# Optimization experiments

Hardware: AMD Instinct MI355X
Metric: run time of the kernel (lower is better)

Reference implementation:

```python
import jax, jax.numpy as jnp
import numpy as np

B, S_SRC, S_TRG = 128, 512, 128
VIN, VOUT = 128, 128
E, H = 128, 256          # embed, encoder hidden
HD = 2 * H               # decoder hidden = 512 (concat of bi-dir encoder states)
DENC = 2 * H             # encoder output feature dim = 512


def setup_inputs() -> dict:
    key = jax.random.key(0)
    ks = jax.random.split(key, 20)
    g = lambda k, shape: (jax.random.normal(k, shape, jnp.float32) * 0.05)
    inp = {
        "src": jax.random.randint(ks[0], (B, S_SRC), 0, VIN, jnp.int32),
        "trg": jax.random.randint(ks[1], (B, S_TRG), 0, VOUT, jnp.int32),
        # encoder
        "enc_emb": g(ks[2], (VIN, E)),
        "enc_Wih_f": g(ks[3], (4 * H, E)),
        "enc_Whh_f": g(ks[4], (4 * H, H)),
        "enc_b_f": g(ks[5], (4 * H,)),
        "enc_Wih_b": g(ks[6], (4 * H, E)),
        "enc_Whh_b": g(ks[7], (4 * H, H)),
        "enc_b_b": g(ks[8], (4 * H,)),
        # decoder
        "dec_emb": g(ks[9], (VOUT, E)),
        "dec_Wih": g(ks[10], (4 * HD, E + DENC)),
        "dec_Whh": g(ks[11], (4 * HD, HD)),
        "dec_b": g(ks[12], (4 * HD,)),
        # attention: Linear(dec_hid + enc_dim -> HD), v: Linear(HD -> 1)
        "attn_W": g(ks[13], (HD + DENC, HD)),
        "attn_b": g(ks[14], (HD,)),
        "attn_v": g(ks[15], (HD,)),
        # output projection
        "out_W": g(ks[16], (HD, VOUT)),
        "out_b": g(ks[17], (VOUT,)),
    }
    return inp


def _lstm_cell(h, c, x, Wih, Whh, b):
    gates = x @ Wih.T + h @ Whh.T + b               # [B, 4H]
    i, f, gg, o = jnp.split(gates, 4, axis=-1)       # PyTorch gate order i,f,g,o
    i, f, o = jax.nn.sigmoid(i), jax.nn.sigmoid(f), jax.nn.sigmoid(o)
    c = f * c + i * jnp.tanh(gg)
    h = o * jnp.tanh(c)
    return h, c


def _lstm_scan(xs, Wih, Whh, b, reverse=False):
    # xs: [S, B, E] -> hs: [S, B, H] (time-aligned), plus final (h, c)
    Bn, Hn = xs.shape[1], Whh.shape[1]
    init = (jnp.zeros((Bn, Hn), xs.dtype), jnp.zeros((Bn, Hn), xs.dtype))
    def step(carry, x):
        h, c = _lstm_cell(carry[0], carry[1], x, Wih, Whh, b)
        return (h, c), h
    (h, c), hs = jax.lax.scan(step, init, xs, reverse=reverse)
    return hs, h, c


def reference(src, trg, enc_emb, enc_Wih_f, enc_Whh_f, enc_b_f,
              enc_Wih_b, enc_Whh_b, enc_b_b, dec_emb, dec_Wih, dec_Whh,
              dec_b, attn_W, attn_b, attn_v, out_W, out_b):
    # ----- encoder (bidirectional LSTM) -----
    emb = enc_emb[src]                                # [B, S, E]
    xs = jnp.swapaxes(emb, 0, 1)                      # [S, B, E]
    hs_f, hf, cf = _lstm_scan(xs, enc_Wih_f, enc_Whh_f, enc_b_f, reverse=False)
    hs_b, hb, cb = _lstm_scan(xs, enc_Wih_b, enc_Whh_b, enc_b_b, reverse=True)
    enc_out = jnp.swapaxes(jnp.concatenate([hs_f, hs_b], -1), 0, 1)  # [B, S, 2H]
    hidden = jnp.concatenate([hf, hb], -1)            # [B, HD]  (hidden.view(1,B,-1))
    cell = jnp.concatenate([cf, cb], -1)              # [B, HD]

    # attention linear split: energy = tanh([h, enc] @ W + b)
    Wh, We = attn_W[:HD], attn_W[HD:]
    enc_proj = jnp.einsum("bsd,de->bse", enc_out, We)  # [B, S, HD] precomputed

    def dec_step(carry, tok):
        h, c = carry
        e = jnp.tanh(h[:, None, :] @ Wh + enc_proj + attn_b)     # [B, S, HD]
        scores = jnp.einsum("bse,e->bs", e, attn_v)              # [B, S]
        aw = jax.nn.softmax(scores, axis=1)
        ctx = jnp.einsum("bs,bsd->bd", aw, enc_out)              # [B, DENC]
        x = jnp.concatenate([dec_emb[tok], ctx], -1)             # [B, E+DENC]
        h, c = _lstm_cell(h, c, x, dec_Wih, dec_Whh, dec_b)
        logits = h @ out_W + out_b                               # [B, VOUT]
        return (h, c), logits

    # teacher forcing (ratio=1.0): input at step t is trg[:, t-1], t = 1..T-1
    toks = jnp.swapaxes(trg[:, :-1], 0, 1)            # [T-1, B]
    _, logits = jax.lax.scan(dec_step, (hidden, cell), toks)
    logits = jnp.swapaxes(logits, 0, 1)               # [B, T-1, VOUT]
    outputs = jnp.concatenate(
        [jnp.zeros((src.shape[0], 1, VOUT), logits.dtype), logits], axis=1)
    return outputs
```

## Files before the change

### kernel.cpp

```cpp
#include <hip/hip_runtime.h>


typedef _Float16 f16;
typedef _Float16 half8 __attribute__((ext_vector_type(8)));
typedef float f32x4 __attribute__((ext_vector_type(4)));
typedef char char8v __attribute__((ext_vector_type(8)));

#define MFMA16(a, b, c) __builtin_amdgcn_mfma_f32_16x16x32_f16((a), (b), (c), 0, 0, 0)

#define PSCALE (2.5f / 127.f)
#define PINV   (127.f / 2.5f)

__device__ __forceinline__ float fsig(float x) {
    return __builtin_amdgcn_rcpf(1.f + __expf(-x));
}
__device__ __forceinline__ float ftanh(float x) {
    return 1.f - 2.f * __builtin_amdgcn_rcpf(1.f + __expf(2.f * x));
}
__device__ __forceinline__ int frag_idx(int m, int k, int KS) {
    return (((m >> 4) * KS + (k >> 5)) * 64 + (((k >> 3) & 3) * 16 + (m & 15))) * 8 + (k & 7);
}

__global__ __launch_bounds__(256) void k_prep(
    const float* __restrict__ attn_W, const float* __restrict__ out_W,
    const float* __restrict__ enc_emb,
    const float* __restrict__ wihf, const float* __restrict__ wihb,
    const float* __restrict__ whhf, const float* __restrict__ whhb,
    const float* __restrict__ dec_emb, const float* __restrict__ dec_wih,
    const float* __restrict__ dec_whh,
    f16* __restrict__ WhT_sw, f16* __restrict__ outWT_sw,
    f16* __restrict__ whhf_sw, f16* __restrict__ whhb_sw,
    f16* __restrict__ decwih_sw, f16* __restrict__ decwhh_sw,
    f16* __restrict__ WeT, f16* __restrict__ emb16,
    f16* __restrict__ wihf16, f16* __restrict__ wihb16,
    f16* __restrict__ decemb16, float* __restrict__ out)
{
    long i = (long)blockIdx.x * 256 + threadIdx.x;
    if (i >= 3784704L) return;
    long idx = i;
    if (idx < 262144) {
        int j = idx & 7, lane = (idx >> 3) & 63, c = lane & 15, q = lane >> 4;
        int ks = (idx >> 9) & 15, nt = idx >> 13;
        WhT_sw[idx] = (f16)attn_W[(ks * 32 + q * 8 + j) * 512 + nt * 16 + c];
        return;
    }
    idx -= 262144;
    if (idx < 65536) {
        int j = idx & 7, lane = (idx >> 3) & 63, c = lane & 15, q = lane >> 4;
        int ks = (idx >> 9) & 15, nt = idx >> 13;
        outWT_sw[idx] = (f16)out_W[(ks * 32 + q * 8 + j) * 128 + nt * 16 + c];
        return;
    }
    idx -= 65536;
    if (idx < 262144) {
        int j = idx & 7, lane = (idx >> 3) & 63, c = lane & 15, q = lane >> 4;
        int ks = (idx >> 9) & 7, nt = idx >> 12;
        whhf_sw[idx] = (f16)whhf[(nt * 16 + c) * 256 + ks * 32 + q * 8 + j];
        return;
    }
    idx -= 262144;
    if (idx < 262144) {
        int j = idx & 7, lane = (idx >> 3) & 63, c = lane & 15, q = lane >> 4;
        int ks = (idx >> 9) & 7, nt = idx >> 12;
        whhb_sw[idx] = (f16)whhb[(nt * 16 + c) * 256 + ks * 32 + q * 8 + j];
        return;
    }
    idx -= 262144;
    if (idx < 1310720) {
        int j = idx & 7, lane = (idx >> 3) & 63, c = lane & 15, q = lane >> 4;
        int r2 = idx >> 9; int ks = r2 % 20, nt = r2 / 20;
        decwih_sw[idx] = (f16)dec_wih[(nt * 16 + c) * 640 + ks * 32 + q * 8 + j];
        return;
    }
    idx -= 1310720;
    if (idx < 1048576) {
        int j = idx & 7, lane = (idx >> 3) & 63, c = lane & 15, q = lane >> 4;
        int ks = (idx >> 9) & 15, nt = idx >> 13;
        decwhh_sw[idx] = (f16)dec_whh[(nt * 16 + c) * 512 + ks * 32 + q * 8 + j];
        return;
    }
    idx -= 1048576;
    if (idx < 262144) { int e = idx >> 9, d = idx & 511; WeT[idx] = (f16)attn_W[(512 + d) * 512 + e]; return; }
    idx -= 262144;
    if (idx < 16384)  { emb16[idx] = (f16)enc_emb[idx]; return; }
    idx -= 16384;
    if (idx < 131072) { wihf16[idx] = (f16)wihf[idx]; return; }
    idx -= 131072;
    if (idx < 131072) { wihb16[idx] = (f16)wihb[idx]; return; }
    idx -= 131072;
    if (idx < 16384)  { decemb16[idx] = (f16)dec_emb[idx]; return; }
    idx -= 16384;
    if (idx < 16384)  { int b = idx >> 7, v = idx & 127; out[b * 16384 + v] = 0.f; return; }
}

__global__ __launch_bounds__(256) void k_vocab(
    const f16* __restrict__ emb, const f16* __restrict__ wihf,
    const f16* __restrict__ wihb, const float* __restrict__ bf_,
    const float* __restrict__ bb_, f16* __restrict__ xg_vocab)
{
    int bn = blockIdx.x;
    int tid = threadIdx.x, wave = tid >> 6, lane = tid & 63;
    int col = lane & 15, quad = lane >> 4;
    int wr = wave >> 1, wc = wave & 1;

    f32x4 acc[4][4] = {};
    for (int ks = 0; ks < 4; ++ks) {
        int k0 = ks * 32 + quad * 8;
        half8 a[4], bfr[4];
        for (int i = 0; i < 4; ++i)
            a[i] = *(const half8*)(emb + (wr * 64 + i * 16 + col) * 128 + k0);
        for (int j = 0; j < 4; ++j) {
            int n = bn * 128 + wc * 64 + j * 16 + col;
            const f16* wp = (n < 1024) ? (wihf + n * 128) : (wihb + (n - 1024) * 128);
            bfr[j] = *(const half8*)(wp + k0);
        }
        for (int i = 0; i < 4; ++i)
            for (int j = 0; j < 4; ++j)
                acc[i][j] = MFMA16(a[i], bfr[j], acc[i][j]);
    }
    for (int j = 0; j < 4; ++j) {
        int n = bn * 128 + wc * 64 + j * 16 + col;
        float bias = (n < 1024) ? bf_[n] : bb_[n - 1024];
        for (int i = 0; i < 4; ++i) {
            int vbase = wr * 64 + i * 16 + quad * 4;
            for (int r = 0; r < 4; ++r)
                xg_vocab[(vbase + r) * 2048 + n] = (f16)(acc[i][j][r] + bias);
        }
    }
}

__global__ __launch_bounds__(512, 2) void k_enc(
    const int* __restrict__ src, const f16* __restrict__ xg_vocab,
    const f16* __restrict__ whhf_sw, const f16* __restrict__ whhb_sw,
    f16* __restrict__ enc_out, f16* __restrict__ hdec0, float* __restrict__ c_ws)
{
    int blk = blockIdx.x;
    int dir = blk >> 3, bbase = (blk & 7) * 16;
    int tid = threadIdx.x, wave = tid >> 6, lane = tid & 63;
    int col = lane & 15, quad = lane >> 4;
    const f16* whh = dir ? whhb_sw : whhf_sw;

    __shared__ f16 hb[16][264];
    __shared__ f16 xvb[16][1032];
    __shared__ int stok[16];
    for (int z = tid; z < 16 * 264; z += 512) ((f16*)hb)[z] = (f16)0.f;
    float cc[2][4] = {};

    half8 bst[32];
    #pragma unroll
    for (int g = 0; g < 2; ++g)
        #pragma unroll
        for (int nt = 0; nt < 2; ++nt)
            #pragma unroll
            for (int kk = 0; kk < 8; ++kk) {
                int tile = g * 16 + wave * 2 + nt;
                bst[(g * 2 + nt) * 8 + kk] =
                    *(const half8*)(whh + ((tile * 8 + kk) * 64 + lane) * 8);
            }
    __syncthreads();

    for (int t = 0; t < 512; ++t) {
        int ts = dir ? (511 - t) : t;
        if (tid < 16) stok[tid] = src[(bbase + tid) * 512 + ts];
        half8 a[8];
        #pragma unroll
        for (int kk = 0; kk < 8; ++kk)
            a[kk] = *(const half8*)(&hb[col][kk * 32 + quad * 8]);
        __syncthreads();

        #pragma unroll
        for (int it = 0; it < 4; ++it) {
            int cnk = it * 512 + tid;
            int row = cnk >> 7, off = (cnk & 127) * 8;
            *(half8*)(&xvb[row][off]) =
                *(const half8*)(xg_vocab + stok[row] * 2048 + dir * 1024 + off);
        }

        f32x4 acc[4][2] = {};
        #pragma unroll
        for (int kk = 0; kk < 8; ++kk) {
            half8 bv[4];
            #pragma unroll
            for (int g = 2; g < 4; ++g)
                #pragma unroll
                for (int nt = 0; nt < 2; ++nt) {
                    int tile = g * 16 + wave * 2 + nt;
                    bv[(g - 2) * 2 + nt] =
                        *(const half8*)(whh + ((tile * 8 + kk) * 64 + lane) * 8);
                }
            #pragma unroll
            for (int g = 0; g < 2; ++g)
                #pragma unroll
                for (int nt = 0; nt < 2; ++nt)
                    acc[g][nt] = MFMA16(a[kk], bst[(g * 2 + nt) * 8 + kk], acc[g][nt]);
            #pragma unroll
            for (int g = 2; g < 4; ++g)
                #pragma unroll
                for (int nt = 0; nt < 2; ++nt)
                    acc[g][nt] = MFMA16(a[kk], bv[(g - 2) * 2 + nt], acc[g][nt]);
        }
        __syncthreads();

        #pragma unroll
        for (int nt = 0; nt < 2; ++nt) {
            int hcol = wave * 32 + nt * 16 + col;
            #pragma unroll
            for (int r = 0; r < 4; ++r) {
                int b = quad * 4 + r;
                float gi = (float)xvb[b][0 * 256 + hcol] + acc[0][nt][r];
                float gf = (float)xvb[b][1 * 256 + hcol] + acc[1][nt][r];
                float gg = (float)xvb[b][2 * 256 + hcol] + acc[2][nt][r];
                float go = (float)xvb[b][3 * 256 + hcol] + acc[3][nt][r];
                float ig = fsig(gi), fg = fsig(gf), g2 = ftanh(gg), og = fsig(go);
                float cv = fg * cc[nt][r] + ig * g2;
                cc[nt][r] = cv;
                float h = og * ftanh(cv);
                f16 h16 = (f16)h;
                hb[b][hcol] = h16;
                enc_out[((size_t)(bbase + b) * 512 + ts) * 512 + dir * 256 + hcol] = h16;
            }
        }
        __syncthreads();
    }
    #pragma unroll
    for (int nt = 0; nt < 2; ++nt) {
        int hcol = wave * 32 + nt * 16 + col;
        #pragma unroll
        for (int r = 0; r < 4; ++r) {
            int b = quad * 4 + r;
            int m = bbase + b, k = dir * 256 + hcol;
            hdec0[frag_idx(m, k, 16)] = hb[b][hcol];
            c_ws[m * 512 + k] = cc[nt][r];
        }
    }
}

__global__ __launch_bounds__(256) void k_proj(
    const f16* __restrict__ enc_out, const f16* __restrict__ WeT,
    char* __restrict__ proj8)
{
    int blk = blockIdx.x;
    int bm = blk & 511, bn = blk >> 9;
    int tid = threadIdx.x, wave = tid >> 6, lane = tid & 63;
    int col = lane & 15, quad = lane >> 4;
    int wr = wave >> 1, wc = wave & 1;

    f32x4 acc[4][4] = {};
    for (int ks = 0; ks < 16; ++ks) {
        int k0 = ks * 32 + quad * 8;
        half8 a[4], bfr[4];
        for (int i = 0; i < 4; ++i) {
            int m = bm * 128 + wr * 64 + i * 16 + col;
            a[i] = *(const half8*)(enc_out + (size_t)m * 512 + k0);
        }
        for (int j = 0; j < 4; ++j) {
            int n = bn * 128 + wc * 64 + j * 16 + col;
            bfr[j] = *(const half8*)(WeT + n * 512 + k0);
        }
        for (int i = 0; i < 4; ++i)
            for (int j = 0; j < 4; ++j)
                acc[i][j] = MFMA16(a[i], bfr[j], acc[i][j]);
    }
    for (int j = 0; j < 4; ++j) {
        int n = bn * 128 + wc * 64 + j * 16 + col;
        for (int i = 0; i < 4; ++i) {
            int mbase = bm * 128 + wr * 64 + i * 16 + quad * 4;
            for (int r = 0; r < 4; ++r) {
                float v = acc[i][j][r] * PINV;
                int q = (int)rintf(v);
                q = (q > 127) ? 127 : ((q < -127) ? -127 : q);
                proj8[(size_t)(mbase + r) * 512 + n] = (char)q;
            }
        }
    }
}

__global__ __launch_bounds__(256) void k_qinit(
    const f16* __restrict__ h0_sw, const f16* __restrict__ WhT_sw,
    float* __restrict__ qpart)
{
    int j = blockIdx.x;
    int tid = threadIdx.x, wave = tid >> 6, lane = tid & 63;
    int col = lane & 15, quad = lane >> 4;
    half8 a[2];
    #pragma unroll
    for (int i = 0; i < 2; ++i)
        a[i] = *(const half8*)(h0_sw + (((wave * 2 + i) * 16 + j) * 64 + lane) * 8);
    for (int nt = 0; nt < 32; ++nt) {
        half8 bfr = *(const half8*)(WhT_sw + ((nt * 16 + j) * 64 + lane) * 8);
        f32x4 q0 = {}, q1 = {};
        q0 = MFMA16(a[0], bfr, q0);
        q1 = MFMA16(a[1], bfr, q1);
        #pragma unroll
        for (int r = 0; r < 4; ++r) {
            qpart[(j * 128 + wave * 32 + quad * 4 + r) * 512 + nt * 16 + col] = q0[r];
            qpart[(j * 128 + wave * 32 + 16 + quad * 4 + r) * 512 + nt * 16 + col] = q1[r];
        }
    }
}

__global__ __launch_bounds__(512) void k_att(
    const char* __restrict__ proj8, const f16* __restrict__ enc_out,
    const float* __restrict__ qpart, const float* __restrict__ attn_b,
    const float* __restrict__ attn_v, const int* __restrict__ trg,
    const f16* __restrict__ dec_emb, f16* __restrict__ x_sw,
    float* __restrict__ part_m, float* __restrict__ part_l,
    float* __restrict__ part_ctx, int t)
{
    int blk = blockIdx.x;
    int b = blk >> 1, sh = blk & 1;
    int tid = threadIdx.x, wave = tid >> 6, lane = tid & 63;
    __shared__ float q[512];
    __shared__ float sc[256];
    __shared__ float ctxred[8][512];
    __shared__ float wred[8], wred2[8];

    {
        float s = attn_b[tid];
        #pragma unroll
        for (int jj = 0; jj < 16; ++jj) s += qpart[(jj * 128 + b) * 512 + tid];
        q[tid] = s;
    }
    __syncthreads();

    float qreg[8], vreg[8];
    #pragma unroll
    for (int u = 0; u < 8; ++u) {
        int e = lane * 8 + u;
        qreg[u] = q[e];
        vreg[u] = attn_v[e];
    }
    int sbase = sh * 256;
    for (int ib = 0; ib < 4; ++ib) {
        char8v p[8];
        #pragma unroll
        for (int z = 0; z < 8; ++z) {
            int sl = (ib * 8 + z) * 8 + wave;
            p[z] = *(const char8v*)(proj8 + ((size_t)b * 512 + sbase + sl) * 512 + lane * 8);
        }
        #pragma unroll
        for (int z = 0; z < 8; ++z) {
            int sl = (ib * 8 + z) * 8 + wave;
            float part = 0.f;
            #pragma unroll
            for (int u = 0; u < 8; ++u)
                part += vreg[u] * ftanh(fmaf((float)p[z][u], PSCALE, qreg[u]));
            #pragma unroll
            for (int o = 32; o; o >>= 1) part += __shfl_xor(part, o);
            if (lane == 0) sc[sl] = part;
        }
    }
    __syncthreads();

    float s0 = (tid < 256) ? sc[tid] : -__builtin_inff();
    float mv = s0;
    #pragma unroll
    for (int o = 32; o; o >>= 1) mv = fmaxf(mv, __shfl_xor(mv, o));
    if (lane == 0) wred[wave] = mv;
    __syncthreads();
    float M = wred[0];
    #pragma unroll
    for (int w = 1; w < 8; ++w) M = fmaxf(M, wred[w]);
    float e0 = (tid < 256) ? __expf(s0 - M) : 0.f;
    if (tid < 256) sc[tid] = e0;
    float sm = e0;
    #pragma unroll
    for (int o = 32; o; o >>= 1) sm += __shfl_xor(sm, o);
    if (lane == 0) wred2[wave] = sm;
    __syncthreads();
    float lb = wred2[0];
    #pragma unroll
    for (int w = 1; w < 8; ++w) lb += wred2[w];

    float a8[8] = {};
    for (int ib = 0; ib < 4; ++ib) {
        half8 ev[8];
        float wgt[8];
        #pragma unroll
        for (int z = 0; z < 8; ++z) {
            int sl = (ib * 8 + z) * 8 + wave;
            ev[z] = *(const half8*)(enc_out + ((size_t)b * 512 + sbase + sl) * 512 + lane * 8);
            wgt[z] = sc[sl];
        }
        #pragma unroll
        for (int z = 0; z < 8; ++z)
            #pragma unroll
            for (int u = 0; u < 8; ++u) a8[u] += wgt[z] * (float)ev[z][u];
    }
    #pragma unroll
    for (int u = 0; u < 8; ++u) ctxred[wave][lane * 8 + u] = a8[u];
    __syncthreads();
    float cp = 0.f;
    #pragma unroll
    for (int w = 0; w < 8; ++w) cp += ctxred[w][tid];
    part_ctx[(size_t)blk * 512 + tid] = cp;
    if (tid == 0) { part_m[blk] = M; part_l[blk] = lb; }

    if (sh == 0 && tid < 128) {
        int tok = trg[b * 128 + t];
        x_sw[frag_idx(b, tid, 20)] = dec_emb[tok * 128 + tid];
    }
}

__global__ __launch_bounds__(256) void k_gates(
    f16* __restrict__ x_sw, const f16* __restrict__ hprev_sw,
    const f16* __restrict__ wih_sw, const f16* __restrict__ whh_sw,
    const float* __restrict__ dec_b, float* __restrict__ c_ws,
    f16* __restrict__ hnext_sw, f16* __restrict__ hhist_sw,
    const f16* __restrict__ WhT_sw, float* __restrict__ qpart,
    const float* __restrict__ part_m, const float* __restrict__ part_l,
    const float* __restrict__ part_ctx, int t)
{
    int jb = blockIdx.x;
    int j = jb >> 1, mh = jb & 1;
    int tid = threadIdx.x, wave = tid >> 6, lane = tid & 63;
    int col = lane & 15, quad = lane >> 4;
    __shared__ f16 hsl[64][40];
    __shared__ float gm[64][2];

    if (tid < 64) {
        int bb = mh * 64 + tid;
        float m0 = part_m[bb * 2 + 0], m1 = part_m[bb * 2 + 1];
        float l0 = part_l[bb * 2 + 0], l1 = part_l[bb * 2 + 1];
        float M = fmaxf(m0, m1);
        float g0 = __expf(m0 - M), g1 = __expf(m1 - M);
        float inv = 1.f / (g0 * l0 + g1 * l1);
        gm[tid][0] = g0 * inv;
        gm[tid][1] = g1 * inv;
    }
    __syncthreads();
    for (int z = tid; z < 32768; z += 256) {
        int lr = z >> 9, d = z & 511;
        int bb = mh * 64 + lr;
        float c = gm[lr][0] * part_ctx[(size_t)(bb * 2 + 0) * 512 + d]
                + gm[lr][1] * part_ctx[(size_t)(bb * 2 + 1) * 512 + d];
        x_sw[frag_idx(bb, 128 + d, 20)] = (f16)c;
    }
    __syncthreads();

    f32x4 acc[8] = {};
    for (int ks = 0; ks < 36; ++ks) {
        int mtile = mh * 4 + wave;
        half8 a = (ks < 20)
            ? *(const half8*)(x_sw + ((mtile * 20 + ks) * 64 + lane) * 8)
            : *(const half8*)(hprev_sw + ((mtile * 16 + (ks - 20)) * 64 + lane) * 8);
        half8 bv[8];
        #pragma unroll
        for (int jt = 0; jt < 8; ++jt) {
            int g = jt >> 1, u2 = jt & 1;
            int ntile = g * 32 + j * 2 + u2;
            bv[jt] = (ks < 20)
                ? *(const half8*)(wih_sw + ((ntile * 20 + ks) * 64 + lane) * 8)
                : *(const half8*)(whh_sw + ((ntile * 16 + (ks - 20)) * 64 + lane) * 8);
        }
        #pragma unroll
        for (int jt = 0; jt < 8; ++jt)
            acc[jt] = MFMA16(a, bv[jt], acc[jt]);
    }
    float bias[8];
    #pragma unroll
    for (int jt = 0; jt < 8; ++jt) {
        int g = jt >> 1, u2 = jt & 1;
        bias[jt] = dec_b[g * 512 + j * 32 + u2 * 16 + col];
    }
    #pragma unroll
    for (int r = 0; r < 4; ++r) {
        int lb = wave * 16 + quad * 4 + r;
        int bb = mh * 64 + lb;
        #pragma unroll
        for (int u2 = 0; u2 < 2; ++u2) {
            int hl = u2 * 16 + col, hcol = j * 32 + hl;
            float gi = acc[0 + u2][r] + bias[0 + u2];
            float gf = acc[2 + u2][r] + bias[2 + u2];
            float gg = acc[4 + u2][r] + bias[4 + u2];
            float go = acc[6 + u2][r] + bias[6 + u2];
            float ig = fsig(gi), fg = fsig(gf), g2 = ftanh(gg), og = fsig(go);
            float cv = fg * c_ws[bb * 512 + hcol] + ig * g2;
            c_ws[bb * 512 + hcol] = cv;
            float h = og * ftanh(cv);
            f16 h16 = (f16)h;
            int fidx = frag_idx(bb, hcol, 16);
            hnext_sw[fidx] = h16;
            hhist_sw[t * 65536 + fidx] = h16;
            hsl[lb][hl] = h16;
        }
    }
    half8 aq = *(const half8*)(&hsl[wave * 16 + col][quad * 8]);
    for (int nt = 0; nt < 32; ++nt) {
        half8 bq = *(const half8*)(WhT_sw + ((nt * 16 + j) * 64 + lane) * 8);
        f32x4 q0 = {};
        q0 = MFMA16(aq, bq, q0);
        #pragma unroll
        for (int r = 0; r < 4; ++r)
            qpart[(j * 128 + mh * 64 + wave * 16 + quad * 4 + r) * 512 + nt * 16 + col] = q0[r];
    }
}

__global__ __launch_bounds__(256) void k_logits(
    const f16* __restrict__ hhist_sw, const f16* __restrict__ outWT_sw,
    const float* __restrict__ out_b, float* __restrict__ out)
{
    int bt = blockIdx.x;
    int tid = threadIdx.x, wave = tid >> 6, lane = tid & 63;
    int col = lane & 15, quad = lane >> 4;
    f32x4 acc[2][8] = {};
    for (int ks = 0; ks < 16; ++ks) {
        half8 a[2];
        #pragma unroll
        for (int i = 0; i < 2; ++i)
            a[i] = *(const half8*)(hhist_sw + bt * 65536 + (((wave * 2 + i) * 16 + ks) * 64 + lane) * 8);
        half8 bv[8];
        #pragma unroll
        for (int jt = 0; jt < 8; ++jt)
            bv[jt] = *(const half8*)(outWT_sw + ((jt * 16 + ks) * 64 + lane) * 8);
        #pragma unroll
        for (int jt = 0; jt < 8; ++jt) {
            acc[0][jt] = MFMA16(a[0], bv[jt], acc[0][jt]);
            acc[1][jt] = MFMA16(a[1], bv[jt], acc[1][jt]);
        }
    }
    #pragma unroll
    for (int jt = 0; jt < 8; ++jt) {
        float bias = out_b[jt * 16 + col];
        #pragma unroll
        for (int i = 0; i < 2; ++i)
            #pragma unroll
            for (int r = 0; r < 4; ++r) {
                int br = wave * 32 + i * 16 + quad * 4 + r;
                out[br * 16384 + (bt + 1) * 128 + jt * 16 + col] = acc[i][jt][r] + bias;
            }
    }
}

extern "C" void kernel_launch(void* const* d_in, const int* in_sizes, int n_in,
                              void* d_out, int out_size, void* d_ws, size_t ws_size,
                              hipStream_t stream)
{
    (void)in_sizes; (void)n_in; (void)out_size;
    if (ws_size < 130000000) return;

    const int*   src     = (const int*)d_in[0];
    const int*   trg     = (const int*)d_in[1];
    const float* enc_emb = (const float*)d_in[2];
    const float* wihf    = (const float*)d_in[3];
    const float* whhf    = (const float*)d_in[4];
    const float* bf_     = (const float*)d_in[5];
    const float* wihb    = (const float*)d_in[6];
    const float* whhb    = (const float*)d_in[7];
    const float* bb_     = (const float*)d_in[8];
    const float* dec_emb = (const float*)d_in[9];
    const float* dec_wih = (const float*)d_in[10];
    const float* dec_whh = (const float*)d_in[11];
    const float* dec_b   = (const float*)d_in[12];
    const float* attn_W  = (const float*)d_in[13];
    const float* attn_b  = (const float*)d_in[14];
    const float* attn_v  = (const float*)d_in[15];
    const float* out_W   = (const float*)d_in[16];
    const float* out_b   = (const float*)d_in[17];
    float* out = (float*)d_out;

    char* p = (char*)d_ws;
    auto carve = [&](size_t n) { char* r = p; p += ((n + 255) & ~(size_t)255); return r; };
    f16*   enc_out   = (f16*)  carve(67108864);
    char*  proj8     = (char*) carve(33554432);
    f16*   WhT_sw    = (f16*)  carve(524288);
    f16*   WeT       = (f16*)  carve(524288);
    f16*   outWT_sw  = (f16*)  carve(131072);
    f16*   emb16     = (f16*)  carve(32768);
    f16*   wihf16    = (f16*)  carve(262144);
    f16*   wihb16    = (f16*)  carve(262144);
    f16*   whhf_sw   = (f16*)  carve(524288);
    f16*   whhb_sw   = (f16*)  carve(524288);
    f16*   decemb16  = (f16*)  carve(32768);
    f16*   decwih_sw = (f16*)  carve(2621440);
    f16*   decwhh_sw = (f16*)  carve(2097152);
    float* qpart     = (float*)carve(4194304);
    f16*   hdec0     = (f16*)  carve(131072);
    f16*   hdec1     = (f16*)  carve(131072);
    float* c_ws      = (float*)carve(262144);
    f16*   x_sw      = (f16*)  carve(163840);
    f16*   hhist_sw  = (f16*)  carve(16646144);
    f16*   xg_vocab  = (f16*)  carve(524288);
    float* part_m    = (float*)carve(2048);
    float* part_l    = (float*)carve(2048);
    float* part_ctx  = (float*)carve(524288);

    k_prep<<<14784, 256, 0, stream>>>(attn_W, out_W, enc_emb, wihf, wihb, whhf, whhb,
                                      dec_emb, dec_wih, dec_whh,
                                      WhT_sw, outWT_sw, whhf_sw, whhb_sw,
                                      decwih_sw, decwhh_sw, WeT, emb16,
                                      wihf16, wihb16, decemb16, out);
    k_vocab<<<16, 256, 0, stream>>>(emb16, wihf16, wihb16, bf_, bb_, xg_vocab);
    k_enc<<<16, 512, 0, stream>>>(src, xg_vocab, whhf_sw, whhb_sw, enc_out, hdec0, c_ws);
    k_proj<<<2048, 256, 0, stream>>>(enc_out, WeT, proj8);
    k_qinit<<<16, 256, 0, stream>>>(hdec0, WhT_sw, qpart);
    for (int t = 0; t < 127; ++t) {
        k_att<<<256, 512, 0, stream>>>(proj8, enc_out, qpart, attn_b, attn_v,
                                       trg, decemb16, x_sw, part_m, part_l,
                                       part_ctx, t);
        f16* hin  = (t & 1) ? hdec1 : hdec0;
        f16* hout = (t & 1) ? hdec0 : hdec1;
        k_gates<<<32, 256, 0, stream>>>(x_sw, hin, decwih_sw, decwhh_sw, dec_b,
                                        c_ws, hout, hhist_sw, WhT_sw, qpart,
                                        part_m, part_l, part_ctx, t);
    }
    k_logits<<<127, 256, 0, stream>>>(hhist_sw, outWT_sw, out_b, out);
}
```

Baseline: 13.06 ms.

## Fuse decoder attention and gate kernels into one persistent kernel with grid barriers

```diff
diff --git a/kernel.cpp b/kernel.cpp
--- a/kernel.cpp
+++ b/kernel.cpp
@@ -19,6 +19,23 @@
 }
 __device__ __forceinline__ int frag_idx(int m, int k, int KS) {
     return (((m >> 4) * KS + (k >> 5)) * 64 + (((k >> 3) & 3) * 16 + (m & 15))) * 8 + (k & 7);
+}
+
+__device__ __forceinline__ void gridbar(int* cnt, int* gen, int nblk) {
+    __syncthreads();
+    if (threadIdx.x == 0) {
+        int g = __hip_atomic_load(gen, __ATOMIC_RELAXED, __HIP_MEMORY_SCOPE_AGENT);
+        int v = __hip_atomic_fetch_add(cnt, 1, __ATOMIC_RELEASE, __HIP_MEMORY_SCOPE_AGENT);
+        if (v == nblk - 1) {
+            __hip_atomic_store(cnt, 0, __ATOMIC_RELAXED, __HIP_MEMORY_SCOPE_AGENT);
+            __hip_atomic_fetch_add(gen, 1, __ATOMIC_RELEASE, __HIP_MEMORY_SCOPE_AGENT);
+        } else {
+            while (__hip_atomic_load(gen, __ATOMIC_RELAXED, __HIP_MEMORY_SCOPE_AGENT) == g)
+                __builtin_amdgcn_s_sleep(2);
+        }
+        __builtin_amdgcn_fence(__ATOMIC_ACQUIRE, "agent");
+    }
+    __syncthreads();
 }
 
 __global__ __launch_bounds__(256) void k_prep(
@@ -33,10 +50,11 @@
     f16* __restrict__ decwih_sw, f16* __restrict__ decwhh_sw,
     f16* __restrict__ WeT, f16* __restrict__ emb16,
     f16* __restrict__ wihf16, f16* __restrict__ wihb16,
-    f16* __restrict__ decemb16, float* __restrict__ out)
+    f16* __restrict__ decemb16, float* __restrict__ out,
+    int* __restrict__ syncb)
 {
     long i = (long)blockIdx.x * 256 + threadIdx.x;
-    if (i >= 3784704L) return;
+    if (i >= 3784768L) return;
     long idx = i;
     if (idx < 262144) {
         int j = idx & 7, lane = (idx >> 3) & 63, c = lane & 15, q = lane >> 4;
@@ -91,6 +109,8 @@
     if (idx < 16384)  { decemb16[idx] = (f16)dec_emb[idx]; return; }
     idx -= 16384;
     if (idx < 16384)  { int b = idx >> 7, v = idx & 127; out[b * 16384 + v] = 0.f; return; }
+    idx -= 16384;
+    if (idx < 64)     { syncb[idx] = 0; return; }
 }
 
 __global__ __launch_bounds__(256) void k_vocab(
@@ -299,200 +319,211 @@
     }
 }
 
-__global__ __launch_bounds__(512) void k_att(
+__global__ __launch_bounds__(512, 2) void k_dec(
     const char* __restrict__ proj8, const f16* __restrict__ enc_out,
-    const float* __restrict__ qpart, const float* __restrict__ attn_b,
+    float* __restrict__ qpart, const float* __restrict__ attn_b,
     const float* __restrict__ attn_v, const int* __restrict__ trg,
-    const f16* __restrict__ dec_emb, f16* __restrict__ x_sw,
+    const f16* __restrict__ decemb, f16* __restrict__ x_sw,
+    const f16* __restrict__ wih_sw, const f16* __restrict__ whh_sw,
+    const float* __restrict__ dec_b, float* __restrict__ c_ws,
+    f16* __restrict__ hd0, f16* __restrict__ hd1, f16* __restrict__ hhist_sw,
+    const f16* __restrict__ WhT_sw,
     float* __restrict__ part_m, float* __restrict__ part_l,
-    float* __restrict__ part_ctx, int t)
+    float* __restrict__ part_ctx, int* __restrict__ syncb)
 {
     int blk = blockIdx.x;
     int b = blk >> 1, sh = blk & 1;
     int tid = threadIdx.x, wave = tid >> 6, lane = tid & 63;
+    int col = lane & 15, quad = lane >> 4;
+    int nblk = gridDim.x;
+    int* cnt = syncb;
+    int* gen = syncb + 16;
+
     __shared__ float q[512];
     __shared__ float sc[256];
     __shared__ float ctxred[8][512];
     __shared__ float wred[8], wred2[8];
-
-    {
-        float s = attn_b[tid];
-        #pragma unroll
-        for (int jj = 0; jj < 16; ++jj) s += qpart[(jj * 128 + b) * 512 + tid];
-        q[tid] = s;
-    }
-    __syncthreads();
-
-    float qreg[8], vreg[8];
-    #pragma unroll
-    for (int u = 0; u < 8; ++u) {
-        int e = lane * 8 + u;
-        qreg[u] = q[e];
-        vreg[u] = attn_v[e];
-    }
-    int sbase = sh * 256;
-    for (int ib = 0; ib < 4; ++ib) {
-        char8v p[8];
-        #pragma unroll
-        for (int z = 0; z < 8; ++z) {
-            int sl = (ib * 8 + z) * 8 + wave;
-            p[z] = *(const char8v*)(proj8 + ((size_t)b * 512 + sbase + sl) * 512 + lane * 8);
-        }
-        #pragma unroll
-        for (int z = 0; z < 8; ++z) {
-            int sl = (ib * 8 + z) * 8 + wave;
-            float part = 0.f;
-            #pragma unroll
-            for (int u = 0; u < 8; ++u)
-                part += vreg[u] * ftanh(fmaf((float)p[z][u], PSCALE, qreg[u]));
-            #pragma unroll
-            for (int o = 32; o; o >>= 1) part += __shfl_xor(part, o);
-            if (lane == 0) sc[sl] = part;
-        }
-    }
-    __syncthreads();
-
-    float s0 = (tid < 256) ? sc[tid] : -__builtin_inff();
-    float mv = s0;
-    #pragma unroll
-    for (int o = 32; o; o >>= 1) mv = fmaxf(mv, __shfl_xor(mv, o));
-    if (lane == 0) wred[wave] = mv;
-    __syncthreads();
-    float M = wred[0];
-    #pragma unroll
-    for (int w = 1; w < 8; ++w) M = fmaxf(M, wred[w]);
-    float e0 = (tid < 256) ? __expf(s0 - M) : 0.f;
-    if (tid < 256) sc[tid] = e0;
-    float sm = e0;
-    #pragma unroll
-    for (int o = 32; o; o >>= 1) sm += __shfl_xor(sm, o);
-    if (lane == 0) wred2[wave] = sm;
-    __syncthreads();
-    float lb = wred2[0];
-    #pragma unroll
-    for (int w = 1; w < 8; ++w) lb += wred2[w];
-
-    float a8[8] = {};
-    for (int ib = 0; ib < 4; ++ib) {
-        half8 ev[8];
-        float wgt[8];
-        #pragma unroll
-        for (int z = 0; z < 8; ++z) {
-            int sl = (ib * 8 + z) * 8 + wave;
-            ev[z] = *(const half8*)(enc_out + ((size_t)b * 512 + sbase + sl) * 512 + lane * 8);
-            wgt[z] = sc[sl];
-        }
-        #pragma unroll
-        for (int z = 0; z < 8; ++z)
-            #pragma unroll
-            for (int u = 0; u < 8; ++u) a8[u] += wgt[z] * (float)ev[z][u];
-    }
-    #pragma unroll
-    for (int u = 0; u < 8; ++u) ctxred[wave][lane * 8 + u] = a8[u];
-    __syncthreads();
-    float cp = 0.f;
-    #pragma unroll
-    for (int w = 0; w < 8; ++w) cp += ctxred[w][tid];
-    part_ctx[(size_t)blk * 512 + tid] = cp;
-    if (tid == 0) { part_m[blk] = M; part_l[blk] = lb; }
-
-    if (sh == 0 && tid < 128) {
-        int tok = trg[b * 128 + t];
-        x_sw[frag_idx(b, tid, 20)] = dec_emb[tok * 128 + tid];
-    }
-}
-
-__global__ __launch_bounds__(256) void k_gates(
-    f16* __restrict__ x_sw, const f16* __restrict__ hprev_sw,
-    const f16* __restrict__ wih_sw, const f16* __restrict__ whh_sw,
-    const float* __restrict__ dec_b, float* __restrict__ c_ws,
-    f16* __restrict__ hnext_sw, f16* __restrict__ hhist_sw,
-    const f16* __restrict__ WhT_sw, float* __restrict__ qpart,
-    const float* __restrict__ part_m, const float* __restrict__ part_l,
-    const float* __restrict__ part_ctx, int t)
-{
-    int jb = blockIdx.x;
-    int j = jb >> 1, mh = jb & 1;
-    int tid = threadIdx.x, wave = tid >> 6, lane = tid & 63;
-    int col = lane & 15, quad = lane >> 4;
     __shared__ f16 hsl[64][40];
     __shared__ float gm[64][2];
 
-    if (tid < 64) {
-        int bb = mh * 64 + tid;
-        float m0 = part_m[bb * 2 + 0], m1 = part_m[bb * 2 + 1];
-        float l0 = part_l[bb * 2 + 0], l1 = part_l[bb * 2 + 1];
-        float M = fmaxf(m0, m1);
-        float g0 = __expf(m0 - M), g1 = __expf(m1 - M);
-        float inv = 1.f / (g0 * l0 + g1 * l1);
-        gm[tid][0] = g0 * inv;
-        gm[tid][1] = g1 * inv;
-    }
-    __syncthreads();
-    for (int z = tid; z < 32768; z += 256) {
-        int lr = z >> 9, d = z & 511;
-        int bb = mh * 64 + lr;
-        float c = gm[lr][0] * part_ctx[(size_t)(bb * 2 + 0) * 512 + d]
-                + gm[lr][1] * part_ctx[(size_t)(bb * 2 + 1) * 512 + d];
-        x_sw[frag_idx(bb, 128 + d, 20)] = (f16)c;
-    }
-    __syncthreads();
-
-    f32x4 acc[8] = {};
-    for (int ks = 0; ks < 36; ++ks) {
-        int mtile = mh * 4 + wave;
-        half8 a = (ks < 20)
-            ? *(const half8*)(x_sw + ((mtile * 20 + ks) * 64 + lane) * 8)
-            : *(const half8*)(hprev_sw + ((mtile * 16 + (ks - 20)) * 64 + lane) * 8);
-        half8 bv[8];
+    int gj = blk >> 1, gmh = blk & 1;
+    float bias[8];
+    if (blk < 32) {
         #pragma unroll
         for (int jt = 0; jt < 8; ++jt) {
             int g = jt >> 1, u2 = jt & 1;
-            int ntile = g * 32 + j * 2 + u2;
-            bv[jt] = (ks < 20)
-                ? *(const half8*)(wih_sw + ((ntile * 20 + ks) * 64 + lane) * 8)
-                : *(const half8*)(whh_sw + ((ntile * 16 + (ks - 20)) * 64 + lane) * 8);
-        }
-        #pragma unroll
-        for (int jt = 0; jt < 8; ++jt)
-            acc[jt] = MFMA16(a, bv[jt], acc[jt]);
-    }
-    float bias[8];
+            bias[jt] = dec_b[g * 512 + gj * 32 + u2 * 16 + col];
+        }
+    }
+    float vreg[8];
     #pragma unroll
-    for (int jt = 0; jt < 8; ++jt) {
-        int g = jt >> 1, u2 = jt & 1;
-        bias[jt] = dec_b[g * 512 + j * 32 + u2 * 16 + col];
-    }
-    #pragma unroll
-    for (int r = 0; r < 4; ++r) {
-        int lb = wave * 16 + quad * 4 + r;
-        int bb = mh * 64 + lb;
-        #pragma unroll
-        for (int u2 = 0; u2 < 2; ++u2) {
-            int hl = u2 * 16 + col, hcol = j * 32 + hl;
-            float gi = acc[0 + u2][r] + bias[0 + u2];
-            float gf = acc[2 + u2][r] + bias[2 + u2];
-            float gg = acc[4 + u2][r] + bias[4 + u2];
-            float go = acc[6 + u2][r] + bias[6 + u2];
-            float ig = fsig(gi), fg = fsig(gf), g2 = ftanh(gg), og = fsig(go);
-            float cv = fg * c_ws[bb * 512 + hcol] + ig * g2;
-            c_ws[bb * 512 + hcol] = cv;
-            float h = og * ftanh(cv);
-            f16 h16 = (f16)h;
-            int fidx = frag_idx(bb, hcol, 16);
-            hnext_sw[fidx] = h16;
-            hhist_sw[t * 65536 + fidx] = h16;
-            hsl[lb][hl] = h16;
-        }
-    }
-    half8 aq = *(const half8*)(&hsl[wave * 16 + col][quad * 8]);
-    for (int nt = 0; nt < 32; ++nt) {
-        half8 bq = *(const half8*)(WhT_sw + ((nt * 16 + j) * 64 + lane) * 8);
-        f32x4 q0 = {};
-        q0 = MFMA16(aq, bq, q0);
-        #pragma unroll
-        for (int r = 0; r < 4; ++r)
-            qpart[(j * 128 + mh * 64 + wave * 16 + quad * 4 + r) * 512 + nt * 16 + col] = q0[r];
+    for (int u = 0; u < 8; ++u) vreg[u] = attn_v[lane * 8 + u];
+    int sbase = sh * 256;
+
+    for (int t = 0; t < 127; ++t) {
+        {
+            float s = attn_b[tid];
+            #pragma unroll
+            for (int jj = 0; jj < 16; ++jj) s += qpart[(jj * 128 + b) * 512 + tid];
+            q[tid] = s;
+        }
+        __syncthreads();
+
+        float qreg[8];
+        #pragma unroll
+        for (int u = 0; u < 8; ++u) qreg[u] = q[lane * 8 + u];
+
+        for (int ib = 0; ib < 4; ++ib) {
+            char8v p[8];
+            #pragma unroll
+            for (int z = 0; z < 8; ++z) {
+                int sl = (ib * 8 + z) * 8 + wave;
+                p[z] = *(const char8v*)(proj8 + ((size_t)b * 512 + sbase + sl) * 512 + lane * 8);
+            }
+            #pragma unroll
+            for (int z = 0; z < 8; ++z) {
+                int sl = (ib * 8 + z) * 8 + wave;
+                float part = 0.f;
+                #pragma unroll
+                for (int u = 0; u < 8; ++u)
+                    part += vreg[u] * ftanh(fmaf((float)p[z][u], PSCALE, qreg[u]));
+                #pragma unroll
+                for (int o = 32; o; o >>= 1) part += __shfl_xor(part, o);
+                if (lane == 0) sc[sl] = part;
+            }
+        }
+        __syncthreads();
+
+        float s0 = (tid < 256) ? sc[tid] : -__builtin_inff();
+        float mv = s0;
+        #pragma unroll
+        for (int o = 32; o; o >>= 1) mv = fmaxf(mv, __shfl_xor(mv, o));
+        if (lane == 0) wred[wave] = mv;
+        __syncthreads();
+        float M = wred[0];
+        #pragma unroll
+        for (int w = 1; w < 8; ++w) M = fmaxf(M, wred[w]);
+        float e0 = (tid < 256) ? __expf(s0 - M) : 0.f;
+        if (tid < 256) sc[tid] = e0;
+        float sm = e0;
+        #pragma unroll
+        for (int o = 32; o; o >>= 1) sm += __shfl_xor(sm, o);
+        if (lane == 0) wred2[wave] = sm;
+        __syncthreads();
+        float lb2 = wred2[0];
+        #pragma unroll
+        for (int w = 1; w < 8; ++w) lb2 += wred2[w];
+
+        float a8[8] = {};
+        for (int ib = 0; ib < 4; ++ib) {
+            half8 ev[8];
+            float wgt[8];
+            #pragma unroll
+            for (int z = 0; z < 8; ++z) {
+                int sl = (ib * 8 + z) * 8 + wave;
+                ev[z] = *(const half8*)(enc_out + ((size_t)b * 512 + sbase + sl) * 512 + lane * 8);
+                wgt[z] = sc[sl];
+            }
+            #pragma unroll
+            for (int z = 0; z < 8; ++z)
+                #pragma unroll
+                for (int u = 0; u < 8; ++u) a8[u] += wgt[z] * (float)ev[z][u];
+        }
+        #pragma unroll
+        for (int u = 0; u < 8; ++u) ctxred[wave][lane * 8 + u] = a8[u];
+        __syncthreads();
+        float cp = 0.f;
+        #pragma unroll
+        for (int w = 0; w < 8; ++w) cp += ctxred[w][tid];
+        part_ctx[(size_t)blk * 512 + tid] = cp;
+        if (tid == 0) { part_m[blk] = M; part_l[blk] = lb2; }
+
+        if (sh == 0 && tid < 128) {
+            int tok = trg[b * 128 + t];
+            x_sw[frag_idx(b, tid, 20)] = decemb[tok * 128 + tid];
+        }
+
+        gridbar(cnt, gen, nblk);
+
+        if (blk < 32 && tid < 64) {
+            int bb = gmh * 64 + tid;
+            float m0 = part_m[bb * 2 + 0], m1 = part_m[bb * 2 + 1];
+            float l0 = part_l[bb * 2 + 0], l1 = part_l[bb * 2 + 1];
+            float Mx = fmaxf(m0, m1);
+            float g0 = __expf(m0 - Mx), g1 = __expf(m1 - Mx);
+            float inv = 1.f / (g0 * l0 + g1 * l1);
+            gm[tid][0] = g0 * inv;
+            gm[tid][1] = g1 * inv;
+        }
+        __syncthreads();
+        if (blk < 32) {
+            for (int z = tid; z < 32768; z += 512) {
+                int lr = z >> 9, d = z & 511;
+                int bb = gmh * 64 + lr;
+                float c = gm[lr][0] * part_ctx[(size_t)(bb * 2 + 0) * 512 + d]
+                        + gm[lr][1] * part_ctx[(size_t)(bb * 2 + 1) * 512 + d];
+                x_sw[frag_idx(bb, 128 + d, 20)] = (f16)c;
+            }
+        }
+        __syncthreads();
+
+        if (blk < 32 && wave < 4) {
+            const f16* hprev = (t & 1) ? hd1 : hd0;
+            f16* hnext = (t & 1) ? hd0 : hd1;
+
+            f32x4 acc[8] = {};
+            for (int ks = 0; ks < 36; ++ks) {
+                int mtile = gmh * 4 + wave;
+                half8 a = (ks < 20)
+                    ? *(const half8*)(x_sw + ((mtile * 20 + ks) * 64 + lane) * 8)
+                    : *(const half8*)(hprev + ((mtile * 16 + (ks - 20)) * 64 + lane) * 8);
+                half8 bv[8];
+                #pragma unroll
+                for (int jt = 0; jt < 8; ++jt) {
+                    int g = jt >> 1, u2 = jt & 1;
+                    int ntile = g * 32 + gj * 2 + u2;
+                    bv[jt] = (ks < 20)
+                        ? *(const half8*)(wih_sw + ((ntile * 20 + ks) * 64 + lane) * 8)
+                        : *(const half8*)(whh_sw + ((ntile * 16 + (ks - 20)) * 64 + lane) * 8);
+                }
+                #pragma unroll
+                for (int jt = 0; jt < 8; ++jt)
+                    acc[jt] = MFMA16(a, bv[jt], acc[jt]);
+            }
+            #pragma unroll
+            for (int r = 0; r < 4; ++r) {
+                int lr = wave * 16 + quad * 4 + r;
+                int bb = gmh * 64 + lr;
+                #pragma unroll
+                for (int u2 = 0; u2 < 2; ++u2) {
+                    int hl = u2 * 16 + col, hcol = gj * 32 + hl;
+                    float gi = acc[0 + u2][r] + bias[0 + u2];
+                    float gf = acc[2 + u2][r] + bias[2 + u2];
+                    float gg = acc[4 + u2][r] + bias[4 + u2];
+                    float go = acc[6 + u2][r] + bias[6 + u2];
+                    float ig = fsig(gi), fg = fsig(gf), g2 = ftanh(gg), og = fsig(go);
+                    float cv = fg * c_ws[bb * 512 + hcol] + ig * g2;
+                    c_ws[bb * 512 + hcol] = cv;
+                    float h = og * ftanh(cv);
+                    f16 h16 = (f16)h;
+                    int fidx = frag_idx(bb, hcol, 16);
+                    hnext[fidx] = h16;
+                    hhist_sw[t * 65536 + fidx] = h16;
+                    hsl[lr][hl] = h16;
+                }
+            }
+            half8 aq = *(const half8*)(&hsl[wave * 16 + col][quad * 8]);
+            for (int nt = 0; nt < 32; ++nt) {
+                half8 bq = *(const half8*)(WhT_sw + ((nt * 16 + gj) * 64 + lane) * 8);
+                f32x4 q0 = {};
+                q0 = MFMA16(aq, bq, q0);
+                #pragma unroll
+                for (int r = 0; r < 4; ++r)
+                    qpart[(gj * 128 + gmh * 64 + wave * 16 + quad * 4 + r) * 512 + nt * 16 + col] = q0[r];
+            }
+        }
+
+        gridbar(cnt, gen, nblk);
     }
 }
 
@@ -584,25 +615,20 @@
     float* part_m    = (float*)carve(2048);
     float* part_l    = (float*)carve(2048);
     float* part_ctx  = (float*)carve(524288);
-
-    k_prep<<<14784, 256, 0, stream>>>(attn_W, out_W, enc_emb, wihf, wihb, whhf, whhb,
+    int*   syncb     = (int*)  carve(256);
+
+    k_prep<<<14785, 256, 0, stream>>>(attn_W, out_W, enc_emb, wihf, wihb, whhf, whhb,
                                       dec_emb, dec_wih, dec_whh,
                                       WhT_sw, outWT_sw, whhf_sw, whhb_sw,
                                       decwih_sw, decwhh_sw, WeT, emb16,
-                                      wihf16, wihb16, decemb16, out);
+                                      wihf16, wihb16, decemb16, out, syncb);
     k_vocab<<<16, 256, 0, stream>>>(emb16, wihf16, wihb16, bf_, bb_, xg_vocab);
     k_enc<<<16, 512, 0, stream>>>(src, xg_vocab, whhf_sw, whhb_sw, enc_out, hdec0, c_ws);
     k_proj<<<2048, 256, 0, stream>>>(enc_out, WeT, proj8);
     k_qinit<<<16, 256, 0, stream>>>(hdec0, WhT_sw, qpart);
-    for (int t = 0; t < 127; ++t) {
-        k_att<<<256, 512, 0, stream>>>(proj8, enc_out, qpart, attn_b, attn_v,
-                                       trg, decemb16, x_sw, part_m, part_l,
-                                       part_ctx, t);
-        f16* hin  = (t & 1) ? hdec1 : hdec0;
-        f16* hout = (t & 1) ? hdec0 : hdec1;
-        k_gates<<<32, 256, 0, stream>>>(x_sw, hin, decwih_sw, decwhh_sw, dec_b,
-                                        c_ws, hout, hhist_sw, WhT_sw, qpart,
-                                        part_m, part_l, part_ctx, t);
-    }
+    k_dec<<<256, 512, 0, stream>>>(proj8, enc_out, qpart, attn_b, attn_v, trg,
+                                   decemb16, x_sw, decwih_sw, decwhh_sw, dec_b,
+                                   c_ws, hdec0, hdec1, hhist_sw, WhT_sw,
+                                   part_m, part_l, part_ctx, syncb);
     k_logits<<<127, 256, 0, stream>>>(hhist_sw, outWT_sw, out_b, out);
 }
```

Measured after the change: 20.45 ms. +56.6%, slower.
